# Performance work log

Hardware: AMD Instinct MI355X
Metric: run time of the kernel (lower is better)

## Reference

```python
import jax, jax.numpy as jnp
import numpy as np

MARGIN = 0.2
SCALE = 30.0

def setup_inputs() -> dict:
    key = jax.random.key(0)
    k1, k2 = jax.random.split(key)
    B, D, C = 8192, 512, 100
    embeddings = jax.random.normal(k1, (B, D), dtype=jnp.float32)
    labels = jax.random.randint(k2, (B,), 0, C, dtype=jnp.int64)
    return {"embeddings": embeddings, "labels": labels}

def reference(embeddings, labels):
    # Cosine similarity via one GEMM: normalize rows once, then n @ n.T.
    # (torch F.cosine_similarity uses eps=1e-8 on norms)
    norms = jnp.maximum(jnp.linalg.norm(embeddings, axis=1, keepdims=True), 1e-8)
    n = embeddings / norms                      # [B, D]
    sim = n @ n.T                               # [B, B]
    pos_mask = labels[:, None] == labels[None, :]  # includes diagonal, as in original
    e = jnp.exp(SCALE * (sim - MARGIN))         # [B, B]
    pos_sum = jnp.sum(jnp.where(pos_mask, e, 0.0))
    neg_sum = jnp.sum(jnp.where(pos_mask, 0.0, e))
    loss = jnp.log1p(neg_sum / pos_sum)
    return loss
```

## Files before the change

kernel.cpp:

```cpp
#include <hip/hip_runtime.h>
#include <hip/hip_bf16.h>
#include <math.h>


#define BDIM 8192
#define DDIM 512
#define MARGIN 0.2f
#define SCALE 30.0f

#define BM 128
#define BN 128
#define BK 32
#define NTILES (BDIM / BM)

typedef __hip_bfloat16 bf16;
using f32x4  = __attribute__((ext_vector_type(4))) float;
using bf16x8 = __attribute__((ext_vector_type(8))) short;

#define GLOAD_LDS16(gp, lp)                                                    \
    __builtin_amdgcn_global_load_lds(                                          \
        (const __attribute__((address_space(1))) unsigned int*)(gp),           \
        (__attribute__((address_space(3))) unsigned int*)(lp), 16, 0, 0)

__global__ void norm_rows_kernel(const float* __restrict__ emb,
                                 bf16* __restrict__ nout) {
    const int row = blockIdx.x;
    const int t = threadIdx.x;
    const float2 v = ((const float2*)(emb + (size_t)row * DDIM))[t];
    float ss = v.x * v.x + v.y * v.y;
    #pragma unroll
    for (int off = 32; off > 0; off >>= 1) ss += __shfl_down(ss, off, 64);
    __shared__ float partial[4];
    const int wave = t >> 6, lane = t & 63;
    if (lane == 0) partial[wave] = ss;
    __syncthreads();
    __shared__ float s_inv;
    if (t == 0) {
        float tot = partial[0] + partial[1] + partial[2] + partial[3];
        float nrm = fmaxf(sqrtf(tot), 1e-8f);
        s_inv = 1.0f / nrm;
    }
    __syncthreads();
    const float inv = s_inv;
    __hip_bfloat162 h2;
    h2.x = __float2bfloat16(v.x * inv);
    h2.y = __float2bfloat16(v.y * inv);
    ((__hip_bfloat162*)(nout + (size_t)row * DDIM))[t] = h2;
}

__global__ __launch_bounds__(256)
void gemm_loss_kernel(const bf16* __restrict__ nmat,
                      const int* __restrict__ labels,
                      double* __restrict__ accum ) {
    const int bj = blockIdx.x;
    const int bi = blockIdx.y;
    if (bj < bi) return;

    __shared__ short As[BM * BK];
    __shared__ short Bs[BN * BK];
    __shared__ int   lr[BM];
    __shared__ int   lc[BN];
    __shared__ double red[8];

    const int t = threadIdx.x;
    const int wave = t >> 6;
    const int lane = t & 63;

    if (t < 128) lr[t] = labels[bi * BM + t];
    else         lc[t - 128] = labels[bj * BN + (t - 128)];

    const int wr = wave >> 1;
    const int wc = wave & 1;

    f32x4 acc[4][4] = {};

    const int srow = (lane >> 2);
    const int scol = (lane & 3) * 8;
    const bf16* gA0 = nmat + (size_t)(bi * BM + wave * 16 + srow) * DDIM + scol;
    const bf16* gA1 = gA0 + (size_t)64 * DDIM;
    const bf16* gB0 = nmat + (size_t)(bj * BN + wave * 16 + srow) * DDIM + scol;
    const bf16* gB1 = gB0 + (size_t)64 * DDIM;
    short* lA0 = As + (wave * 16) * BK;
    short* lA1 = As + (64 + wave * 16) * BK;
    short* lB0 = Bs + (wave * 16) * BK;
    short* lB1 = Bs + (64 + wave * 16) * BK;

    const int frow = lane & 15;
    const int koff = (lane >> 4) * 8;

    #pragma unroll 1
    for (int kt = 0; kt < DDIM / BK; ++kt) {
        const int k0 = kt * BK;
        GLOAD_LDS16(gA0 + k0, lA0);
        GLOAD_LDS16(gA1 + k0, lA1);
        GLOAD_LDS16(gB0 + k0, lB0);
        GLOAD_LDS16(gB1 + k0, lB1);
        __syncthreads();

        bf16x8 af[4], bfr[4];
        #pragma unroll
        for (int m = 0; m < 4; ++m)
            af[m] = *(const bf16x8*)&As[(wr * 64 + m * 16 + frow) * BK + koff];
        #pragma unroll
        for (int nn = 0; nn < 4; ++nn)
            bfr[nn] = *(const bf16x8*)&Bs[(wc * 64 + nn * 16 + frow) * BK + koff];
        #pragma unroll
        for (int m = 0; m < 4; ++m)
            #pragma unroll
            for (int nn = 0; nn < 4; ++nn)
                acc[m][nn] = __builtin_amdgcn_mfma_f32_16x16x32_bf16(
                    af[m], bfr[nn], acc[m][nn], 0, 0, 0);
        __syncthreads();
    }

    const float k_scale = SCALE;
    float posf = 0.0f, negf = 0.0f;
    const int rbase = wr * 64 + (lane >> 4) * 4;
    const int cbase = wc * 64 + (lane & 15);
    #pragma unroll
    for (int m = 0; m < 4; ++m) {
        #pragma unroll
        for (int nn = 0; nn < 4; ++nn) {
            const int lcol = cbase + nn * 16;
            const int ljv = lc[lcol];
            #pragma unroll
            for (int r = 0; r < 4; ++r) {
                const int lrow = rbase + m * 16 + r;
                const float sim = acc[m][nn][r];
                const float e = __expf(k_scale * (sim - MARGIN));
                if (lr[lrow] == ljv) posf += e; else negf += e;
            }
        }
    }

    double dp = (double)posf, dn = (double)negf;
    #pragma unroll
    for (int off = 32; off > 0; off >>= 1) {
        dp += __shfl_down(dp, off, 64);
        dn += __shfl_down(dn, off, 64);
    }
    if (lane == 0) { red[wave * 2] = dp; red[wave * 2 + 1] = dn; }
    __syncthreads();
    if (t == 0) {
        const double w = (bi == bj) ? 1.0 : 2.0;
        double p = (red[0] + red[2]) + (red[4] + red[6]);
        double q = (red[1] + red[3]) + (red[5] + red[7]);
        atomicAdd(&accum[0], p * w);
        atomicAdd(&accum[1], q * w);
    }
}

__global__ void finalize_kernel(const double* __restrict__ accum,
                                float* __restrict__ out) {
    if (threadIdx.x == 0 && blockIdx.x == 0) {
        const double r = accum[1] / accum[0];
        out[0] = (float)log1p(r);
    }
}

extern "C" void kernel_launch(void* const* d_in, const int* in_sizes, int n_in,
                              void* d_out, int out_size, void* d_ws, size_t ws_size,
                              hipStream_t stream) {
    const float* emb   = (const float*)d_in[0];
    const int* labels  = (const int*)d_in[1];
    float* out         = (float*)d_out;

    double* accum = (double*)d_ws;
    bf16* nmat    = (bf16*)((char*)d_ws + 256);

    hipMemsetAsync(d_ws, 0, 256, stream);
    norm_rows_kernel<<<BDIM, 256, 0, stream>>>(emb, nmat);
    dim3 grid(NTILES, NTILES);
    gemm_loss_kernel<<<grid, 256, 0, stream>>>(nmat, labels, accum);
    finalize_kernel<<<1, 64, 0, stream>>>(accum, out);
}
```

Baseline: 156.7 us.

## Double-buffer GEMM K-loop, use triangular grid, and vectorize row normalization

The GEMM loads each K tile into one of two LDS buffers while the other is consumed, using explicit vmcnt waits and barriers. The 64x64 grid, where blocks below the diagonal exit immediately, becomes a 1D launch over upper-triangle tiles only, with the tile index recovered by a sqrt formula. The normalization kernel now handles one row per wave with float4 loads and a shuffle reduction instead of one row per 256-thread block. Launch bounds request 4 blocks per SM; the double LDS buffers and manual waitcnt handling add occupancy pressure and correctness risk.

New measurement: 143.8 us. 8.2% less time.

```diff
diff --git a/kernel.cpp b/kernel.cpp
--- a/kernel.cpp
+++ b/kernel.cpp
@@ -11,55 +11,63 @@
 #define BM 128
 #define BN 128
 #define BK 32
+#define NKT (DDIM / BK)
 #define NTILES (BDIM / BM)
+#define NBLK (NTILES * (NTILES + 1) / 2)
 
 typedef __hip_bfloat16 bf16;
 using f32x4  = __attribute__((ext_vector_type(4))) float;
 using bf16x8 = __attribute__((ext_vector_type(8))) short;
+using us8    = __attribute__((ext_vector_type(8))) unsigned short;
 
 #define GLOAD_LDS16(gp, lp)                                                    \
     __builtin_amdgcn_global_load_lds(                                          \
         (const __attribute__((address_space(1))) unsigned int*)(gp),           \
         (__attribute__((address_space(3))) unsigned int*)(lp), 16, 0, 0)
 
-__global__ void norm_rows_kernel(const float* __restrict__ emb,
-                                 bf16* __restrict__ nout) {
-    const int row = blockIdx.x;
-    const int t = threadIdx.x;
-    const float2 v = ((const float2*)(emb + (size_t)row * DDIM))[t];
-    float ss = v.x * v.x + v.y * v.y;
-    #pragma unroll
-    for (int off = 32; off > 0; off >>= 1) ss += __shfl_down(ss, off, 64);
-    __shared__ float partial[4];
-    const int wave = t >> 6, lane = t & 63;
-    if (lane == 0) partial[wave] = ss;
-    __syncthreads();
-    __shared__ float s_inv;
-    if (t == 0) {
-        float tot = partial[0] + partial[1] + partial[2] + partial[3];
-        float nrm = fmaxf(sqrtf(tot), 1e-8f);
-        s_inv = 1.0f / nrm;
-    }
-    __syncthreads();
-    const float inv = s_inv;
-    __hip_bfloat162 h2;
-    h2.x = __float2bfloat16(v.x * inv);
-    h2.y = __float2bfloat16(v.y * inv);
-    ((__hip_bfloat162*)(nout + (size_t)row * DDIM))[t] = h2;
+__device__ __forceinline__ unsigned short f2bf(float x) {
+    union { bf16 h; unsigned short u; } c;
+    c.h = __float2bfloat16(x);
+    return c.u;
 }
 
 __global__ __launch_bounds__(256)
+void norm_rows_kernel(const float* __restrict__ emb, bf16* __restrict__ nout) {
+    const int row  = blockIdx.x * 4 + (threadIdx.x >> 6);
+    const int lane = threadIdx.x & 63;
+    const float4* src = (const float4*)(emb + (size_t)row * DDIM) + lane * 2;
+    const float4 a = src[0];
+    const float4 b = src[1];
+    float ss = a.x * a.x + a.y * a.y + a.z * a.z + a.w * a.w
+             + b.x * b.x + b.y * b.y + b.z * b.z + b.w * b.w;
+    #pragma unroll
+    for (int off = 1; off < 64; off <<= 1) ss += __shfl_xor(ss, off, 64);
+    const float inv = 1.0f / fmaxf(sqrtf(ss), 1e-8f);
+
+    float v[8] = { a.x, a.y, a.z, a.w, b.x, b.y, b.z, b.w };
+    us8 o;
+    #pragma unroll
+    for (int i = 0; i < 8; ++i) o[i] = f2bf(v[i] * inv);
+    *((us8*)(nout + (size_t)row * DDIM) + lane) = o;
+}
+
+__global__ __launch_bounds__(256, 4)
 void gemm_loss_kernel(const bf16* __restrict__ nmat,
                       const int* __restrict__ labels,
                       double* __restrict__ accum ) {
-    const int bj = blockIdx.x;
-    const int bi = blockIdx.y;
-    if (bj < bi) return;
+    const int l = blockIdx.x;
+    auto off = [](int b) { return (129 * b - b * b) >> 1; };
+    int bi = (int)((129.0 - sqrt(16641.0 - 8.0 * (double)l)) * 0.5);
+    if (bi < 0) bi = 0;
+    if (bi > 63) bi = 63;
+    while (bi > 0 && off(bi) > l) --bi;
+    while (off(bi + 1) <= l) ++bi;
+    const int bj = bi + (l - off(bi));
 
-    __shared__ short As[BM * BK];
-    __shared__ short Bs[BN * BK];
-    __shared__ int   lr[BM];
-    __shared__ int   lc[BN];
+    __shared__ alignas(16) short As[2][BM * BK];
+    __shared__ alignas(16) short Bs[2][BN * BK];
+    __shared__ int    lr[BM];
+    __shared__ int    lc[BN];
     __shared__ double red[8];
 
     const int t = threadIdx.x;
@@ -80,40 +88,55 @@
     const bf16* gA1 = gA0 + (size_t)64 * DDIM;
     const bf16* gB0 = nmat + (size_t)(bj * BN + wave * 16 + srow) * DDIM + scol;
     const bf16* gB1 = gB0 + (size_t)64 * DDIM;
-    short* lA0 = As + (wave * 16) * BK;
-    short* lA1 = As + (64 + wave * 16) * BK;
-    short* lB0 = Bs + (wave * 16) * BK;
-    short* lB1 = Bs + (64 + wave * 16) * BK;
 
     const int frow = lane & 15;
     const int koff = (lane >> 4) * 8;
 
-    #pragma unroll 1
-    for (int kt = 0; kt < DDIM / BK; ++kt) {
+    auto STAGE = [&](int buf, int kt) {
         const int k0 = kt * BK;
-        GLOAD_LDS16(gA0 + k0, lA0);
-        GLOAD_LDS16(gA1 + k0, lA1);
-        GLOAD_LDS16(gB0 + k0, lB0);
-        GLOAD_LDS16(gB1 + k0, lB1);
-        __syncthreads();
-
+        GLOAD_LDS16(gA0 + k0, &As[buf][(wave * 16) * BK]);
+        GLOAD_LDS16(gA1 + k0, &As[buf][(64 + wave * 16) * BK]);
+        GLOAD_LDS16(gB0 + k0, &Bs[buf][(wave * 16) * BK]);
+        GLOAD_LDS16(gB1 + k0, &Bs[buf][(64 + wave * 16) * BK]);
+    };
+    auto COMPUTE = [&](int buf) {
         bf16x8 af[4], bfr[4];
         #pragma unroll
         for (int m = 0; m < 4; ++m)
-            af[m] = *(const bf16x8*)&As[(wr * 64 + m * 16 + frow) * BK + koff];
+            af[m] = *(const bf16x8*)&As[buf][(wr * 64 + m * 16 + frow) * BK + koff];
         #pragma unroll
-        for (int nn = 0; nn < 4; ++nn)
-            bfr[nn] = *(const bf16x8*)&Bs[(wc * 64 + nn * 16 + frow) * BK + koff];
+        for (int n = 0; n < 4; ++n)
+            bfr[n] = *(const bf16x8*)&Bs[buf][(wc * 64 + n * 16 + frow) * BK + koff];
         #pragma unroll
         for (int m = 0; m < 4; ++m)
             #pragma unroll
-            for (int nn = 0; nn < 4; ++nn)
-                acc[m][nn] = __builtin_amdgcn_mfma_f32_16x16x32_bf16(
-                    af[m], bfr[nn], acc[m][nn], 0, 0, 0);
-        __syncthreads();
+            for (int n = 0; n < 4; ++n)
+                acc[m][n] = __builtin_amdgcn_mfma_f32_16x16x32_bf16(
+                    af[m], bfr[n], acc[m][n], 0, 0, 0);
+    };
+
+    STAGE(0, 0);
+    STAGE(1, 1);
+    #pragma unroll 2
+    for (int kt = 0; kt < NKT - 2; ++kt) {
+        asm volatile("s_waitcnt vmcnt(4)" ::: "memory");
+        __builtin_amdgcn_s_barrier();
+        asm volatile("" ::: "memory");
+        COMPUTE(kt & 1);
+        asm volatile("" ::: "memory");
+        __builtin_amdgcn_s_barrier();
+        asm volatile("" ::: "memory");
+        STAGE(kt & 1, kt + 2);
     }
+    asm volatile("s_waitcnt vmcnt(4)" ::: "memory");
+    __builtin_amdgcn_s_barrier();
+    asm volatile("" ::: "memory");
+    COMPUTE((NKT - 2) & 1);
+    asm volatile("s_waitcnt vmcnt(0)" ::: "memory");
+    __builtin_amdgcn_s_barrier();
+    asm volatile("" ::: "memory");
+    COMPUTE((NKT - 1) & 1);
 
-    const float k_scale = SCALE;
     float posf = 0.0f, negf = 0.0f;
     const int rbase = wr * 64 + (lane >> 4) * 4;
     const int cbase = wc * 64 + (lane & 15);
@@ -121,23 +144,21 @@
     for (int m = 0; m < 4; ++m) {
         #pragma unroll
         for (int nn = 0; nn < 4; ++nn) {
-            const int lcol = cbase + nn * 16;
-            const int ljv = lc[lcol];
+            const int ljv = lc[cbase + nn * 16];
             #pragma unroll
             for (int r = 0; r < 4; ++r) {
-                const int lrow = rbase + m * 16 + r;
                 const float sim = acc[m][nn][r];
-                const float e = __expf(k_scale * (sim - MARGIN));
-                if (lr[lrow] == ljv) posf += e; else negf += e;
+                const float e = __expf(fmaf(sim, SCALE, -SCALE * MARGIN));
+                if (lr[rbase + m * 16 + r] == ljv) posf += e; else negf += e;
             }
         }
     }
 
     double dp = (double)posf, dn = (double)negf;
     #pragma unroll
-    for (int off = 32; off > 0; off >>= 1) {
-        dp += __shfl_down(dp, off, 64);
-        dn += __shfl_down(dn, off, 64);
+    for (int o = 32; o > 0; o >>= 1) {
+        dp += __shfl_down(dp, o, 64);
+        dn += __shfl_down(dn, o, 64);
     }
     if (lane == 0) { red[wave * 2] = dp; red[wave * 2 + 1] = dn; }
     __syncthreads();
@@ -169,8 +190,7 @@
     bf16* nmat    = (bf16*)((char*)d_ws + 256);
 
     hipMemsetAsync(d_ws, 0, 256, stream);
-    norm_rows_kernel<<<BDIM, 256, 0, stream>>>(emb, nmat);
-    dim3 grid(NTILES, NTILES);
-    gemm_loss_kernel<<<grid, 256, 0, stream>>>(nmat, labels, accum);
+    norm_rows_kernel<<<BDIM / 4, 256, 0, stream>>>(emb, nmat);
+    gemm_loss_kernel<<<NBLK, 256, 0, stream>>>(nmat, labels, accum);
     finalize_kernel<<<1, 64, 0, stream>>>(accum, out);
 }
```
